# Performance work log

Measured on AMD Instinct MI355X. Metric: run time of the kernel, lower is better.

## Reference

```python
import jax, jax.numpy as jnp
import numpy as np

N_HASHES = 4
N_BUCKETS = 8
NUM_HEADS = 8
LN_EPS = 1e-5


def layer_norm(x, g, b):
    m = jnp.mean(x, axis=-1, keepdims=True)
    v = jnp.mean(jnp.square(x - m), axis=-1, keepdims=True)
    return (x - m) * jax.lax.rsqrt(v + LN_EPS) * g + b


def setup_inputs() -> dict:
    key = jax.random.key(0)
    ks = jax.random.split(key, 8)
    B, N, C = 16, 8192, 256
    dff = 4 * C
    w = 0.05  # weight init scale
    return {
        'x': jax.random.normal(ks[0], (B, N, C), jnp.float32),
        'rotations': jax.random.normal(ks[1], (1, C, N_HASHES, N_BUCKETS // 2), jnp.float32),
        'norm1_g': jnp.ones((C,), jnp.float32),
        'norm1_b': jnp.zeros((C,), jnp.float32),
        'q_w': jax.random.normal(ks[2], (C, C), jnp.float32) * w,
        'kv_w': jax.random.normal(ks[3], (C, 2 * C), jnp.float32) * w,
        'norm2_g': jnp.ones((C,), jnp.float32),
        'norm2_b': jnp.zeros((C,), jnp.float32),
        'fc1_w': jax.random.normal(ks[4], (C, dff), jnp.float32) * w,
        'fc1_b': jnp.zeros((dff,), jnp.float32),
        'fc2_w': jax.random.normal(ks[5], (dff, C), jnp.float32) * w,
        'fc2_b': jnp.zeros((C,), jnp.float32),
    }


def reference(x, rotations, norm1_g, norm1_b, q_w, kv_w, norm2_g, norm2_b, fc1_w, fc1_b, fc2_w, fc2_b):
    B, N, C = x.shape
    H = NUM_HEADS
    Dh = C // H
    scale = Dh ** -0.5

    x_ = layer_norm(x, norm1_g, norm1_b)

    # q: [B, H, N, Dh]
    q = (x_ @ q_w).reshape(B, N, H, Dh).transpose(0, 2, 1, 3)

    # --- hash_vectors: LSH bucket assignment + scatter-pool ---
    # rotated: [B, n_hashes, N, n_buckets//2] -> concat with negation -> n_buckets
    rotated = jnp.einsum('btf,fhi->bhti', x_, rotations[0])
    rotated = jnp.concatenate([rotated, -rotated], axis=-1)
    buckets = jnp.argmax(rotated, axis=-1)                      # [B, n_hashes, N]
    one_hot = jax.nn.one_hot(buckets, N_BUCKETS, dtype=x.dtype)  # [B, n_hashes, N, n_buckets]
    sum_buckets = jnp.sum(one_hot, axis=2)                       # [B, n_hashes, n_buckets]
    pooled = jnp.einsum('bnf,bhni->bhif', x_, one_hot)           # [B, n_hashes, n_buckets, C]
    pooled = pooled / (jax.lax.stop_gradient(sum_buckets)[..., None] + 1e-20)
    rp_x = pooled.reshape(B, N_HASHES * N_BUCKETS, C)            # [B, M, C] pooled KV tokens
    sumb = jax.lax.stop_gradient(sum_buckets.reshape(B, N_HASHES * N_BUCKETS))

    # kv: [2, B, H, M, Dh]
    M = N_HASHES * N_BUCKETS
    kv = (rp_x @ kv_w).reshape(B, M, 2, H, Dh).transpose(2, 0, 3, 1, 4)
    k, v = kv[0], kv[1]

    # masked attention over pooled buckets
    attn = jnp.einsum('bhnd,bhmd->bhnm', q, k) * scale           # [B, H, N, M]
    mask = (sumb >= 1)[:, None, None, :]                          # [B, 1, 1, M]
    attn = jnp.where(mask, attn, -jnp.finfo(attn.dtype).max)
    attn = jax.nn.softmax(attn, axis=-1)
    out = jnp.einsum('bhnm,bhmd->bnhd', attn, v).reshape(B, N, C)
    x = x + out

    # MLP block (GELU is exact erf, matching torch nn.GELU default)
    y = layer_norm(x, norm2_g, norm2_b)
    h = jax.nn.gelu(y @ fc1_w + fc1_b, approximate=False)
    y = h @ fc2_w + fc2_b
    return x + y
```

## Files before the change

kernel.cpp:

```cpp
#include <hip/hip_runtime.h>
#include <hip/hip_bf16.h>
#include <float.h>
#include <math.h>

#define Bn   16
#define Nn   8192
#define Cn   256
#define Hn   8
#define DHn  32
#define Mn   32
#define DFFn 1024
#define TOK  64

typedef __attribute__((ext_vector_type(8))) short short8;
typedef __attribute__((ext_vector_type(4))) float f32x4;

__device__ __forceinline__ float bf2f(ushort u) {
    union { unsigned int i; float f; } v; v.i = ((unsigned int)u) << 16; return v.f;
}
__device__ __forceinline__ ushort f2bf(float f) {
    union { float f; unsigned int i; } v; v.f = f;
    unsigned int r = (v.i + 0x7fffu + ((v.i >> 16) & 1u)) >> 16;
    return (ushort)r;
}

__global__ __launch_bounds__(256, 4) void ln1_pool_kernel(
    const float* __restrict__ x, const float* __restrict__ rot,
    const float* __restrict__ g1, const float* __restrict__ b1,
    ushort* __restrict__ xbf, float* __restrict__ pool_part, float* __restrict__ cnt_part)
{
    __shared__ ushort xt[TOK][Cn];
    __shared__ unsigned int idsS[TOK];

    const int tid  = threadIdx.x;
    const int w    = tid >> 6, lane = tid & 63;
    const int o    = lane & 15;
    const int g    = lane >> 4;
    const int fbase = g << 6;

    float rwv[64];
    #pragma unroll
    for (int f = 0; f < 64; ++f) rwv[f] = rot[(fbase + f) * 16 + o];

    const int b  = blockIdx.x >> 7;
    const int n0 = (blockIdx.x & 127) << 6;

    const float4 gv = *(const float4*)&g1[lane * 4];
    const float4 bv = *(const float4*)&b1[lane * 4];

    for (int it = 0; it < TOK / 4; ++it) {
        const int tloc = (it << 2) + w;
        const size_t roff = ((size_t)b * Nn + n0 + tloc) * Cn;
        float4 xv = *(const float4*)&x[roff + lane * 4];
        float s  = xv.x + xv.y + xv.z + xv.w;
        float s2 = xv.x * xv.x + xv.y * xv.y + xv.z * xv.z + xv.w * xv.w;
        #pragma unroll
        for (int msk = 1; msk < 64; msk <<= 1) { s += __shfl_xor(s, msk); s2 += __shfl_xor(s2, msk); }
        float mean = s * (1.f / Cn);
        float var  = s2 * (1.f / Cn) - mean * mean;
        float rr   = rsqrtf(var + 1e-5f);
        float xn[4];
        xn[0] = (xv.x - mean) * rr * gv.x + bv.x;
        xn[1] = (xv.y - mean) * rr * gv.y + bv.y;
        xn[2] = (xv.z - mean) * rr * gv.z + bv.z;
        xn[3] = (xv.w - mean) * rr * gv.w + bv.w;
        ushort4 ub; ub.x = f2bf(xn[0]); ub.y = f2bf(xn[1]); ub.z = f2bf(xn[2]); ub.w = f2bf(xn[3]);
        *(ushort4*)&xbf[roff + lane * 4] = ub;
        *(ushort4*)&xt[tloc][lane * 4] = ub;

        float d = 0.f;
        #pragma unroll
        for (int j = 0; j < 8; ++j) {
            short8 xs = *(const short8*)&xt[tloc][fbase + j * 8];
            #pragma unroll
            for (int u = 0; u < 8; ++u)
                d += bf2f((ushort)xs[u]) * rwv[j * 8 + u];
        }
        d += __shfl_xor(d, 16); d += __shfl_xor(d, 32);

        float d0 = __shfl(d, (lane & 12));
        float d1 = __shfl(d, (lane & 12) | 1);
        float d2 = __shfl(d, (lane & 12) | 2);
        float d3 = __shfl(d, (lane & 12) | 3);
        int bk = 0; float bb = d0;
        if (d1  > bb) { bb = d1;  bk = 1; }
        if (d2  > bb) { bb = d2;  bk = 2; }
        if (d3  > bb) { bb = d3;  bk = 3; }
        if (-d0 > bb) { bb = -d0; bk = 4; }
        if (-d1 > bb) { bb = -d1; bk = 5; }
        if (-d2 > bb) { bb = -d2; bk = 6; }
        if (-d3 > bb) { bb = -d3; bk = 7; }
        const unsigned int bk0 = __shfl(bk, 0), bk1 = __shfl(bk, 4),
                           bk2 = __shfl(bk, 8), bk3 = __shfl(bk, 12);
        if (lane == 0)
            idsS[tloc] = bk0 | (bk1 << 8) | (bk2 << 16) | (bk3 << 24);
    }
    __syncthreads();

    float pool[Mn];
    #pragma unroll
    for (int m = 0; m < Mn; ++m) pool[m] = 0.f;
    for (int t = 0; t < TOK; ++t) {
        const float xv = bf2f(xt[t][tid]);
        const unsigned int idw = idsS[t];
        #pragma unroll
        for (int h = 0; h < 4; ++h) {
            const unsigned int id = (idw >> (8 * h)) & 7u;
            #pragma unroll
            for (int mb = 0; mb < 8; ++mb)
                pool[h * 8 + mb] += (id == (unsigned int)mb) ? xv : 0.f;
        }
    }
    const size_t pbase = (size_t)blockIdx.x * (Mn * Cn);
    #pragma unroll
    for (int m = 0; m < Mn; ++m)
        pool_part[pbase + m * Cn + tid] = pool[m];

    if (tid < Mn) {
        const int h = tid >> 3, mb = tid & 7;
        float c = 0.f;
        for (int t = 0; t < TOK; ++t)
            c += (((idsS[t] >> (8 * h)) & 255u) == (unsigned int)mb) ? 1.f : 0.f;
        cnt_part[blockIdx.x * Mn + tid] = c;
    }
}

__global__ __launch_bounds__(256) void kv_kernel(
    const float* __restrict__ pool_part, const float* __restrict__ cnt_part,
    const float* __restrict__ kv_w, float* __restrict__ kbuf, float* __restrict__ vbuf,
    float* __restrict__ countsF)
{
    __shared__ float rp[Cn];
    const int tid = threadIdx.x;
    const int b = blockIdx.x >> 5;
    const int m = blockIdx.x & 31;

    float acc = 0.f, cnt = 0.f;
    for (int j = 0; j < 128; ++j) {
        const int blk = b * 128 + j;
        acc += pool_part[(size_t)blk * (Mn * Cn) + m * Cn + tid];
        cnt += cnt_part[blk * Mn + m];
    }
    rp[tid] = acc / (cnt + 1e-20f);
    if (tid == 0) countsF[b * Mn + m] = cnt;
    __syncthreads();

    float a0 = 0.f, a1 = 0.f;
    for (int f = 0; f < Cn; ++f) {
        float rv = rp[f];
        a0 += rv * kv_w[f * 512 + tid];
        a1 += rv * kv_w[f * 512 + 256 + tid];
    }
    const int h = tid >> 5, d = tid & 31;
    kbuf[(((size_t)b * Hn + h) * Mn + m) * DHn + d] = a0;
    vbuf[(((size_t)b * Hn + h) * Mn + m) * DHn + d] = a1;
}

template<int EPI>
__global__ __launch_bounds__(256) void gemm_bt(
    const ushort* __restrict__ A, const ushort* __restrict__ Bt,
    const float* __restrict__ bias, const float* __restrict__ resid,
    void* __restrict__ Cp, int Mrows, int Ncols, int K)
{
    __shared__ ushort As[128][40];
    __shared__ ushort Bs[128][40];
    const int tid  = threadIdx.x;
    const int lane = tid & 63;
    const int w    = tid >> 6;
    const int wm   = (w >> 1) << 6;
    const int wn   = (w & 1) << 6;
    const int lr   = lane & 15;
    const int lq   = lane >> 4;
    const int m0   = blockIdx.y << 7;
    const int n0   = blockIdx.x << 7;
    const int srow = tid >> 2;
    const int sch  = (tid & 3) << 3;

    f32x4 acc[4][4];
    #pragma unroll
    for (int i = 0; i < 4; i++)
        #pragma unroll
        for (int j = 0; j < 4; j++)
            acc[i][j] = (f32x4){0.f, 0.f, 0.f, 0.f};

    for (int k0 = 0; k0 < K; k0 += 32) {
        *(uint4*)&As[srow][sch]      = *(const uint4*)&A[(size_t)(m0 + srow) * K + k0 + sch];
        *(uint4*)&As[srow + 64][sch] = *(const uint4*)&A[(size_t)(m0 + srow + 64) * K + k0 + sch];
        *(uint4*)&Bs[srow][sch]      = *(const uint4*)&Bt[(size_t)(n0 + srow) * K + k0 + sch];
        *(uint4*)&Bs[srow + 64][sch] = *(const uint4*)&Bt[(size_t)(n0 + srow + 64) * K + k0 + sch];
        __syncthreads();
        short8 af[4], bfr[4];
        #pragma unroll
        for (int i = 0; i < 4; i++) af[i]  = *(const short8*)&As[wm + i * 16 + lr][lq * 8];
        #pragma unroll
        for (int j = 0; j < 4; j++) bfr[j] = *(const short8*)&Bs[wn + j * 16 + lr][lq * 8];
        #pragma unroll
        for (int i = 0; i < 4; i++)
            #pragma unroll
            for (int j = 0; j < 4; j++)
                acc[i][j] = __builtin_amdgcn_mfma_f32_16x16x32_bf16(af[i], bfr[j], acc[i][j], 0, 0, 0);
        __syncthreads();
    }

    #pragma unroll
    for (int i = 0; i < 4; i++) {
        #pragma unroll
        for (int j = 0; j < 4; j++) {
            const int col = n0 + wn + j * 16 + lr;
            #pragma unroll
            for (int r = 0; r < 4; r++) {
                const int rw = m0 + wm + i * 16 + lq * 4 + r;
                float v = acc[i][j][r];
                if (EPI == 1) { v += bias[col]; v = 0.5f * v * (1.f + erff(v * 0.70710678118654752f)); }
                if (EPI == 2) {
                    v += bias[col] + resid[(size_t)rw * Ncols + col];
                    ((float*)Cp)[(size_t)rw * Ncols + col] = v;
                } else {
                    ((ushort*)Cp)[(size_t)rw * Ncols + col] = f2bf(v);
                }
            }
        }
    }
}

__global__ __launch_bounds__(256) void attn_ln2_kernel(
    const ushort* __restrict__ q, const float* __restrict__ kbuf, const float* __restrict__ vbuf,
    const float* __restrict__ counts, const float* __restrict__ x,
    const float* __restrict__ g2, const float* __restrict__ b2,
    float* __restrict__ x2, ushort* __restrict__ ybf)
{
    __shared__ float kS[Hn * Mn * DHn];
    __shared__ float vS[Hn * Mn * DHn];
    __shared__ float mS[Mn];
    const int tid = threadIdx.x;
    const int b = blockIdx.x >> 5;
    const int n = ((blockIdx.x & 31) << 8) + tid;
    for (int i = tid; i < Hn * Mn * DHn; i += 256) {
        kS[i] = kbuf[(size_t)b * Hn * Mn * DHn + i];
        vS[i] = vbuf[(size_t)b * Hn * Mn * DHn + i];
    }
    if (tid < Mn) mS[tid] = counts[b * Mn + tid];
    __syncthreads();

    const size_t row = (size_t)b * Nn + n;
    float sum = 0.f, sum2 = 0.f;
    for (int h = 0; h < Hn; ++h) {
        float qh[32];
        const ushort* qp = q + row * Cn + h * DHn;
        #pragma unroll
        for (int i = 0; i < 4; ++i) {
            short8 qv = *(const short8*)(qp + i * 8);
            #pragma unroll
            for (int j = 0; j < 8; ++j) qh[i * 8 + j] = bf2f((ushort)qv[j]);
        }
        float p[32]; float mx = -FLT_MAX;
        #pragma unroll
        for (int m = 0; m < 32; ++m) {
            float sv;
            if (mS[m] >= 1.f) {
                sv = 0.f;
                const float* kp = &kS[(h * Mn + m) * DHn];
                #pragma unroll
                for (int dq = 0; dq < 8; ++dq) {
                    float4 k4 = *(const float4*)&kp[dq * 4];
                    sv += qh[dq*4+0]*k4.x + qh[dq*4+1]*k4.y + qh[dq*4+2]*k4.z + qh[dq*4+3]*k4.w;
                }
                sv *= 0.17677669529663687f;
            } else sv = -FLT_MAX;
            p[m] = sv; mx = fmaxf(mx, sv);
        }
        float den = 0.f;
        #pragma unroll
        for (int m = 0; m < 32; ++m) { float e = __expf(p[m] - mx); p[m] = e; den += e; }
        float inv = 1.f / den;
        float o[32];
        #pragma unroll
        for (int dd = 0; dd < 32; ++dd) o[dd] = 0.f;
        #pragma unroll
        for (int m = 0; m < 32; ++m) {
            float pm = p[m];
            const float* vp = &vS[(h * Mn + m) * DHn];
            #pragma unroll
            for (int dq = 0; dq < 8; ++dq) {
                float4 v4 = *(const float4*)&vp[dq * 4];
                o[dq*4+0] += pm*v4.x; o[dq*4+1] += pm*v4.y; o[dq*4+2] += pm*v4.z; o[dq*4+3] += pm*v4.w;
            }
        }
        #pragma unroll
        for (int dq = 0; dq < 8; ++dq) {
            float4 xv = *(const float4*)&x[row * Cn + h * DHn + dq * 4];
            float r0 = xv.x + o[dq*4+0]*inv;
            float r1 = xv.y + o[dq*4+1]*inv;
            float r2 = xv.z + o[dq*4+2]*inv;
            float r3 = xv.w + o[dq*4+3]*inv;
            *(float4*)&x2[row * Cn + h * DHn + dq * 4] = make_float4(r0, r1, r2, r3);
            sum  += r0 + r1 + r2 + r3;
            sum2 += r0*r0 + r1*r1 + r2*r2 + r3*r3;
        }
    }
    float mean = sum * (1.f / Cn);
    float var  = sum2 * (1.f / Cn) - mean * mean;
    float rr   = rsqrtf(var + 1e-5f);
    for (int i = 0; i < Cn / 4; ++i) {
        float4 xv = *(const float4*)&x2[row * Cn + i * 4];
        float4 gv = *(const float4*)&g2[i * 4];
        float4 bv = *(const float4*)&b2[i * 4];
        ushort4 ub;
        ub.x = f2bf((xv.x - mean) * rr * gv.x + bv.x);
        ub.y = f2bf((xv.y - mean) * rr * gv.y + bv.y);
        ub.z = f2bf((xv.z - mean) * rr * gv.z + bv.z);
        ub.w = f2bf((xv.w - mean) * rr * gv.w + bv.w);
        *(ushort4*)&ybf[row * Cn + i * 4] = ub;
    }
}

__global__ void wcast_kernel(const float* __restrict__ W, ushort* __restrict__ Wt, int R, int Cc)
{
    int idx = blockIdx.x * 256 + threadIdx.x;
    if (idx < R * Cc) {
        int r = idx / Cc, c = idx % Cc;
        Wt[(size_t)c * R + r] = f2bf(W[idx]);
    }
}

extern "C" void kernel_launch(void* const* d_in, const int* in_sizes, int n_in,
                              void* d_out, int out_size, void* d_ws, size_t ws_size,
                              hipStream_t stream)
{
    const float* x    = (const float*)d_in[0];
    const float* rot  = (const float*)d_in[1];
    const float* n1g  = (const float*)d_in[2];
    const float* n1b  = (const float*)d_in[3];
    const float* q_w  = (const float*)d_in[4];
    const float* kv_w = (const float*)d_in[5];
    const float* n2g  = (const float*)d_in[6];
    const float* n2b  = (const float*)d_in[7];
    const float* fc1w = (const float*)d_in[8];
    const float* fc1b = (const float*)d_in[9];
    const float* fc2w = (const float*)d_in[10];
    const float* fc2b = (const float*)d_in[11];

    char* ws = (char*)d_ws;
    const size_t XBF_OFF = 0;
    const size_t QBF_OFF = 67108864ull;
    const size_t H_OFF   = 0;
    const size_t X2_OFF  = 268435456ull;
    const size_t PP_OFF  = X2_OFF;
    const size_t CP_OFF  = X2_OFF + 67108864;
    const size_t Y_OFF   = 402653184ull;
    const size_t CT_OFF  = 469762048ull;
    const size_t KB_OFF  = CT_OFF + 4096;
    const size_t VB_OFF  = KB_OFF + 524288;
    const size_t QWT_OFF = VB_OFF + 524288;
    const size_t F1T_OFF = QWT_OFF + 131072;
    const size_t F2T_OFF = F1T_OFF + 524288;

    ushort* xbf    = (ushort*)(ws + XBF_OFF);
    ushort* qbf    = (ushort*)(ws + QBF_OFF);
    ushort* hbf    = (ushort*)(ws + H_OFF);
    float*  x2     = (float*)(ws + X2_OFF);
    float*  ppart  = (float*)(ws + PP_OFF);
    float*  cpart  = (float*)(ws + CP_OFF);
    ushort* ybf    = (ushort*)(ws + Y_OFF);
    float*  countsF= (float*)(ws + CT_OFF);
    float*  kbuf   = (float*)(ws + KB_OFF);
    float*  vbuf   = (float*)(ws + VB_OFF);
    ushort* qwT    = (ushort*)(ws + QWT_OFF);
    ushort* f1T    = (ushort*)(ws + F1T_OFF);
    ushort* f2T    = (ushort*)(ws + F2T_OFF);

    wcast_kernel<<<dim3(256), 256, 0, stream>>>(q_w, qwT, 256, 256);
    wcast_kernel<<<dim3(1024), 256, 0, stream>>>(fc1w, f1T, 256, 1024);
    wcast_kernel<<<dim3(1024), 256, 0, stream>>>(fc2w, f2T, 1024, 256);

    ln1_pool_kernel<<<dim3(Bn * 128), 256, 0, stream>>>(x, rot, n1g, n1b, xbf, ppart, cpart);
    kv_kernel<<<dim3(Bn * Mn), 256, 0, stream>>>(ppart, cpart, kv_w, kbuf, vbuf, countsF);
    gemm_bt<0><<<dim3(2, 1024), 256, 0, stream>>>(xbf, qwT, nullptr, nullptr, qbf, Bn * Nn, Cn, Cn);
    attn_ln2_kernel<<<dim3(Bn * 32), 256, 0, stream>>>(qbf, kbuf, vbuf, countsF, x, n2g, n2b, x2, ybf);
    gemm_bt<1><<<dim3(8, 1024), 256, 0, stream>>>(ybf, f1T, fc1b, nullptr, hbf, Bn * Nn, DFFn, Cn);
    gemm_bt<2><<<dim3(2, 1024), 256, 0, stream>>>(hbf, f2T, fc2b, x2, d_out, Bn * Nn, Cn, DFFn);
}
```

Baseline: 1.095 ms.

## Fold Q projection and K into per-batch score weights, fuse softmax-V-LN2

Precomputes a per-batch matrix W_s = q_w·K^T·scale, so the Q GEMM directly produces attention scores for all heads and the per-token QK dot products disappear. The attention kernel is rewritten so that lanes map to (token pair, head), each lane processes two tokens, and the LayerNorm statistics are reduced with shuffles instead of one thread walking a whole row. The LayerNorm input stays in registers rather than being re-read from global memory. In exchange it adds a small per-batch weight-build kernel and a batched B operand in the GEMM, and the scores are now rounded through bf16 before the softmax.

```diff
diff --git a/kernel.cpp b/kernel.cpp
--- a/kernel.cpp
+++ b/kernel.cpp
@@ -156,11 +156,36 @@
     vbuf[(((size_t)b * Hn + h) * Mn + m) * DHn + d] = a1;
 }
 
+__global__ __launch_bounds__(256) void ws_build_kernel(
+    const float* __restrict__ q_w, const float* __restrict__ kbuf, ushort* __restrict__ WsT)
+{
+    __shared__ float kSh[Mn * DHn];
+    const int tid = threadIdx.x;
+    const int b = blockIdx.x >> 3, h = blockIdx.x & 7;
+    for (int i = tid; i < Mn * DHn; i += 256)
+        kSh[i] = kbuf[((size_t)(b * Hn + h) * Mn) * DHn + i];
+    __syncthreads();
+
+    float qr[32];
+    #pragma unroll
+    for (int i = 0; i < 8; ++i) {
+        float4 v = *(const float4*)&q_w[(size_t)tid * Cn + h * DHn + i * 4];
+        qr[i*4+0] = v.x; qr[i*4+1] = v.y; qr[i*4+2] = v.z; qr[i*4+3] = v.w;
+    }
+    #pragma unroll 4
+    for (int m = 0; m < Mn; ++m) {
+        float s = 0.f;
+        #pragma unroll
+        for (int d = 0; d < DHn; ++d) s += qr[d] * kSh[m * DHn + d];
+        WsT[((size_t)b * Cn + h * Mn + m) * Cn + tid] = f2bf(s * 0.17677669529663687f);
+    }
+}
+
 template<int EPI>
 __global__ __launch_bounds__(256) void gemm_bt(
     const ushort* __restrict__ A, const ushort* __restrict__ Bt,
     const float* __restrict__ bias, const float* __restrict__ resid,
-    void* __restrict__ Cp, int Mrows, int Ncols, int K)
+    void* __restrict__ Cp, int Mrows, int Ncols, int K, int bstride)
 {
     __shared__ ushort As[128][40];
     __shared__ ushort Bs[128][40];
@@ -175,6 +200,7 @@
     const int n0   = blockIdx.x << 7;
     const int srow = tid >> 2;
     const int sch  = (tid & 3) << 3;
+    const ushort* Btb = Bt + (size_t)(m0 >> 13) * (size_t)bstride;
 
     f32x4 acc[4][4];
     #pragma unroll
@@ -186,8 +212,8 @@
     for (int k0 = 0; k0 < K; k0 += 32) {
         *(uint4*)&As[srow][sch]      = *(const uint4*)&A[(size_t)(m0 + srow) * K + k0 + sch];
         *(uint4*)&As[srow + 64][sch] = *(const uint4*)&A[(size_t)(m0 + srow + 64) * K + k0 + sch];
-        *(uint4*)&Bs[srow][sch]      = *(const uint4*)&Bt[(size_t)(n0 + srow) * K + k0 + sch];
-        *(uint4*)&Bs[srow + 64][sch] = *(const uint4*)&Bt[(size_t)(n0 + srow + 64) * K + k0 + sch];
+        *(uint4*)&Bs[srow][sch]      = *(const uint4*)&Btb[(size_t)(n0 + srow) * K + k0 + sch];
+        *(uint4*)&Bs[srow + 64][sch] = *(const uint4*)&Btb[(size_t)(n0 + srow + 64) * K + k0 + sch];
         __syncthreads();
         short8 af[4], bfr[4];
         #pragma unroll
@@ -223,94 +249,134 @@
     }
 }
 
-__global__ __launch_bounds__(256) void attn_ln2_kernel(
-    const ushort* __restrict__ q, const float* __restrict__ kbuf, const float* __restrict__ vbuf,
+#define VSH 1028
+#define GSH 36
+
+__global__ __launch_bounds__(256) void attn2_ln2_kernel(
+    const ushort* __restrict__ S, const float* __restrict__ vbuf,
     const float* __restrict__ counts, const float* __restrict__ x,
     const float* __restrict__ g2, const float* __restrict__ b2,
     float* __restrict__ x2, ushort* __restrict__ ybf)
 {
-    __shared__ float kS[Hn * Mn * DHn];
-    __shared__ float vS[Hn * Mn * DHn];
-    __shared__ float mS[Mn];
+    __shared__ float vS[Hn * VSH];
+    __shared__ float gS[Hn * GSH], bS[Hn * GSH];
+    __shared__ unsigned int mkS;
     const int tid = threadIdx.x;
-    const int b = blockIdx.x >> 5;
-    const int n = ((blockIdx.x & 31) << 8) + tid;
-    for (int i = tid; i < Hn * Mn * DHn; i += 256) {
-        kS[i] = kbuf[(size_t)b * Hn * Mn * DHn + i];
-        vS[i] = vbuf[(size_t)b * Hn * Mn * DHn + i];
-    }
-    if (tid < Mn) mS[tid] = counts[b * Mn + tid];
+    const int b = blockIdx.x >> 6;
+    const int nbase = (blockIdx.x & 63) << 7;
+
+    for (int i = tid; i < Hn * Mn * DHn; i += 256)
+        vS[(i >> 10) * VSH + (i & 1023)] = vbuf[(size_t)b * (Hn * Mn * DHn) + i];
+    gS[(tid >> 5) * GSH + (tid & 31)] = g2[tid];
+    bS[(tid >> 5) * GSH + (tid & 31)] = b2[tid];
+    if (tid == 0) {
+        unsigned int mq = 0;
+        for (int m = 0; m < Mn; ++m) if (counts[b * Mn + m] >= 1.f) mq |= (1u << m);
+        mkS = mq;
+    }
     __syncthreads();
-
-    const size_t row = (size_t)b * Nn + n;
-    float sum = 0.f, sum2 = 0.f;
-    for (int h = 0; h < Hn; ++h) {
-        float qh[32];
-        const ushort* qp = q + row * Cn + h * DHn;
+    const unsigned int mk = mkS;
+    const int w = tid >> 6, lane = tid & 63;
+    const int t8 = lane >> 3, h = lane & 7;
+    const float* vbase = &vS[h * VSH];
+    const float* gp = &gS[h * GSH];
+    const float* bp = &bS[h * GSH];
+
+    for (int it = 0; it < 2; ++it) {
+        const int nl = nbase + it * 64 + w * 16 + t8 * 2;
+        const size_t offA = ((size_t)b * Nn + nl) * Cn + h * DHn;
+
+        float pA[32], pB[32];
         #pragma unroll
         for (int i = 0; i < 4; ++i) {
-            short8 qv = *(const short8*)(qp + i * 8);
-            #pragma unroll
-            for (int j = 0; j < 8; ++j) qh[i * 8 + j] = bf2f((ushort)qv[j]);
-        }
-        float p[32]; float mx = -FLT_MAX;
+            short8 sa = *(const short8*)&S[offA + i * 8];
+            short8 sb = *(const short8*)&S[offA + Cn + i * 8];
+            #pragma unroll
+            for (int j = 0; j < 8; ++j) {
+                pA[i * 8 + j] = bf2f((ushort)sa[j]);
+                pB[i * 8 + j] = bf2f((ushort)sb[j]);
+            }
+        }
+        float mxA = -FLT_MAX, mxB = -FLT_MAX;
         #pragma unroll
         for (int m = 0; m < 32; ++m) {
-            float sv;
-            if (mS[m] >= 1.f) {
-                sv = 0.f;
-                const float* kp = &kS[(h * Mn + m) * DHn];
-                #pragma unroll
-                for (int dq = 0; dq < 8; ++dq) {
-                    float4 k4 = *(const float4*)&kp[dq * 4];
-                    sv += qh[dq*4+0]*k4.x + qh[dq*4+1]*k4.y + qh[dq*4+2]*k4.z + qh[dq*4+3]*k4.w;
-                }
-                sv *= 0.17677669529663687f;
-            } else sv = -FLT_MAX;
-            p[m] = sv; mx = fmaxf(mx, sv);
-        }
-        float den = 0.f;
-        #pragma unroll
-        for (int m = 0; m < 32; ++m) { float e = __expf(p[m] - mx); p[m] = e; den += e; }
-        float inv = 1.f / den;
-        float o[32];
-        #pragma unroll
-        for (int dd = 0; dd < 32; ++dd) o[dd] = 0.f;
+            if (!((mk >> m) & 1u)) { pA[m] = -FLT_MAX; pB[m] = -FLT_MAX; }
+            mxA = fmaxf(mxA, pA[m]); mxB = fmaxf(mxB, pB[m]);
+        }
+        float dA = 0.f, dB = 0.f;
         #pragma unroll
         for (int m = 0; m < 32; ++m) {
-            float pm = p[m];
-            const float* vp = &vS[(h * Mn + m) * DHn];
+            pA[m] = __expf(pA[m] - mxA); dA += pA[m];
+            pB[m] = __expf(pB[m] - mxB); dB += pB[m];
+        }
+        const float iA = 1.f / dA, iB = 1.f / dB;
+
+        float oA[32], oB[32];
+        #pragma unroll
+        for (int i = 0; i < 32; ++i) { oA[i] = 0.f; oB[i] = 0.f; }
+        #pragma unroll
+        for (int m = 0; m < 32; ++m) {
+            const float a = pA[m], c = pB[m];
+            const float* vp = vbase + m * DHn;
             #pragma unroll
             for (int dq = 0; dq < 8; ++dq) {
                 float4 v4 = *(const float4*)&vp[dq * 4];
-                o[dq*4+0] += pm*v4.x; o[dq*4+1] += pm*v4.y; o[dq*4+2] += pm*v4.z; o[dq*4+3] += pm*v4.w;
+                oA[dq*4+0] += a * v4.x; oA[dq*4+1] += a * v4.y;
+                oA[dq*4+2] += a * v4.z; oA[dq*4+3] += a * v4.w;
+                oB[dq*4+0] += c * v4.x; oB[dq*4+1] += c * v4.y;
+                oB[dq*4+2] += c * v4.z; oB[dq*4+3] += c * v4.w;
             }
         }
+
+        float sA = 0.f, s2A = 0.f, sB = 0.f, s2B = 0.f;
         #pragma unroll
         for (int dq = 0; dq < 8; ++dq) {
-            float4 xv = *(const float4*)&x[row * Cn + h * DHn + dq * 4];
-            float r0 = xv.x + o[dq*4+0]*inv;
-            float r1 = xv.y + o[dq*4+1]*inv;
-            float r2 = xv.z + o[dq*4+2]*inv;
-            float r3 = xv.w + o[dq*4+3]*inv;
-            *(float4*)&x2[row * Cn + h * DHn + dq * 4] = make_float4(r0, r1, r2, r3);
-            sum  += r0 + r1 + r2 + r3;
-            sum2 += r0*r0 + r1*r1 + r2*r2 + r3*r3;
-        }
-    }
-    float mean = sum * (1.f / Cn);
-    float var  = sum2 * (1.f / Cn) - mean * mean;
-    float rr   = rsqrtf(var + 1e-5f);
-    for (int i = 0; i < Cn / 4; ++i) {
-        float4 xv = *(const float4*)&x2[row * Cn + i * 4];
-        float4 gv = *(const float4*)&g2[i * 4];
-        float4 bv = *(const float4*)&b2[i * 4];
-        ushort4 ub;
-        ub.x = f2bf((xv.x - mean) * rr * gv.x + bv.x);
-        ub.y = f2bf((xv.y - mean) * rr * gv.y + bv.y);
-        ub.z = f2bf((xv.z - mean) * rr * gv.z + bv.z);
-        ub.w = f2bf((xv.w - mean) * rr * gv.w + bv.w);
-        *(ushort4*)&ybf[row * Cn + i * 4] = ub;
+            float4 xa = *(const float4*)&x[offA + dq * 4];
+            float4 xb = *(const float4*)&x[offA + Cn + dq * 4];
+            float r0 = xa.x + oA[dq*4+0] * iA;
+            float r1 = xa.y + oA[dq*4+1] * iA;
+            float r2 = xa.z + oA[dq*4+2] * iA;
+            float r3 = xa.w + oA[dq*4+3] * iA;
+            float u0 = xb.x + oB[dq*4+0] * iB;
+            float u1 = xb.y + oB[dq*4+1] * iB;
+            float u2 = xb.z + oB[dq*4+2] * iB;
+            float u3 = xb.w + oB[dq*4+3] * iB;
+            *(float4*)&x2[offA + dq * 4]      = make_float4(r0, r1, r2, r3);
+            *(float4*)&x2[offA + Cn + dq * 4] = make_float4(u0, u1, u2, u3);
+            oA[dq*4+0] = r0; oA[dq*4+1] = r1; oA[dq*4+2] = r2; oA[dq*4+3] = r3;
+            oB[dq*4+0] = u0; oB[dq*4+1] = u1; oB[dq*4+2] = u2; oB[dq*4+3] = u3;
+            sA += r0 + r1 + r2 + r3; s2A += r0*r0 + r1*r1 + r2*r2 + r3*r3;
+            sB += u0 + u1 + u2 + u3; s2B += u0*u0 + u1*u1 + u2*u2 + u3*u3;
+        }
+        #pragma unroll
+        for (int msk = 1; msk < 8; msk <<= 1) {
+            sA += __shfl_xor(sA, msk);  s2A += __shfl_xor(s2A, msk);
+            sB += __shfl_xor(sB, msk);  s2B += __shfl_xor(s2B, msk);
+        }
+        const float mA = sA * (1.f / Cn), vA = s2A * (1.f / Cn) - mA * mA;
+        const float rrA = rsqrtf(vA + 1e-5f);
+        const float mB = sB * (1.f / Cn), vB = s2B * (1.f / Cn) - mB * mB;
+        const float rrB = rsqrtf(vB + 1e-5f);
+
+        #pragma unroll
+        for (int dq = 0; dq < 8; dq += 2) {
+            short8 ya, yb;
+            #pragma unroll
+            for (int u = 0; u < 2; ++u) {
+                float4 g4 = *(const float4*)&gp[(dq + u) * 4];
+                float4 b4 = *(const float4*)&bp[(dq + u) * 4];
+                ya[u*4+0] = (short)f2bf((oA[(dq+u)*4+0] - mA) * rrA * g4.x + b4.x);
+                ya[u*4+1] = (short)f2bf((oA[(dq+u)*4+1] - mA) * rrA * g4.y + b4.y);
+                ya[u*4+2] = (short)f2bf((oA[(dq+u)*4+2] - mA) * rrA * g4.z + b4.z);
+                ya[u*4+3] = (short)f2bf((oA[(dq+u)*4+3] - mA) * rrA * g4.w + b4.w);
+                yb[u*4+0] = (short)f2bf((oB[(dq+u)*4+0] - mB) * rrB * g4.x + b4.x);
+                yb[u*4+1] = (short)f2bf((oB[(dq+u)*4+1] - mB) * rrB * g4.y + b4.y);
+                yb[u*4+2] = (short)f2bf((oB[(dq+u)*4+2] - mB) * rrB * g4.z + b4.z);
+                yb[u*4+3] = (short)f2bf((oB[(dq+u)*4+3] - mB) * rrB * g4.w + b4.w);
+            }
+            *(short8*)&ybf[offA + dq * 4]      = ya;
+            *(short8*)&ybf[offA + Cn + dq * 4] = yb;
+        }
     }
 }
 
@@ -342,7 +408,7 @@
 
     char* ws = (char*)d_ws;
     const size_t XBF_OFF = 0;
-    const size_t QBF_OFF = 67108864ull;
+    const size_t S_OFF   = 67108864ull;
     const size_t H_OFF   = 0;
     const size_t X2_OFF  = 268435456ull;
     const size_t PP_OFF  = X2_OFF;
@@ -351,32 +417,31 @@
     const size_t CT_OFF  = 469762048ull;
     const size_t KB_OFF  = CT_OFF + 4096;
     const size_t VB_OFF  = KB_OFF + 524288;
-    const size_t QWT_OFF = VB_OFF + 524288;
-    const size_t F1T_OFF = QWT_OFF + 131072;
+    const size_t F1T_OFF = VB_OFF + 524288;
     const size_t F2T_OFF = F1T_OFF + 524288;
 
     ushort* xbf    = (ushort*)(ws + XBF_OFF);
-    ushort* qbf    = (ushort*)(ws + QBF_OFF);
+    ushort* Sbuf   = (ushort*)(ws + S_OFF);
     ushort* hbf    = (ushort*)(ws + H_OFF);
     float*  x2     = (float*)(ws + X2_OFF);
     float*  ppart  = (float*)(ws + PP_OFF);
     float*  cpart  = (float*)(ws + CP_OFF);
+    ushort* WsT    = (ushort*)(ws + X2_OFF);
     ushort* ybf    = (ushort*)(ws + Y_OFF);
     float*  countsF= (float*)(ws + CT_OFF);
     float*  kbuf   = (float*)(ws + KB_OFF);
     float*  vbuf   = (float*)(ws + VB_OFF);
-    ushort* qwT    = (ushort*)(ws + QWT_OFF);
     ushort* f1T    = (ushort*)(ws + F1T_OFF);
     ushort* f2T    = (ushort*)(ws + F2T_OFF);
 
-    wcast_kernel<<<dim3(256), 256, 0, stream>>>(q_w, qwT, 256, 256);
     wcast_kernel<<<dim3(1024), 256, 0, stream>>>(fc1w, f1T, 256, 1024);
     wcast_kernel<<<dim3(1024), 256, 0, stream>>>(fc2w, f2T, 1024, 256);
 
     ln1_pool_kernel<<<dim3(Bn * 128), 256, 0, stream>>>(x, rot, n1g, n1b, xbf, ppart, cpart);
     kv_kernel<<<dim3(Bn * Mn), 256, 0, stream>>>(ppart, cpart, kv_w, kbuf, vbuf, countsF);
-    gemm_bt<0><<<dim3(2, 1024), 256, 0, stream>>>(xbf, qwT, nullptr, nullptr, qbf, Bn * Nn, Cn, Cn);
-    attn_ln2_kernel<<<dim3(Bn * 32), 256, 0, stream>>>(qbf, kbuf, vbuf, countsF, x, n2g, n2b, x2, ybf);
-    gemm_bt<1><<<dim3(8, 1024), 256, 0, stream>>>(ybf, f1T, fc1b, nullptr, hbf, Bn * Nn, DFFn, Cn);
-    gemm_bt<2><<<dim3(2, 1024), 256, 0, stream>>>(hbf, f2T, fc2b, x2, d_out, Bn * Nn, Cn, DFFn);
-}
+    ws_build_kernel<<<dim3(Bn * Hn), 256, 0, stream>>>(q_w, kbuf, WsT);
+    gemm_bt<0><<<dim3(2, 1024), 256, 0, stream>>>(xbf, WsT, nullptr, nullptr, Sbuf, Bn * Nn, Cn, Cn, Cn * Cn);
+    attn2_ln2_kernel<<<dim3(Bn * 64), 256, 0, stream>>>(Sbuf, vbuf, countsF, x, n2g, n2b, x2, ybf);
+    gemm_bt<1><<<dim3(8, 1024), 256, 0, stream>>>(ybf, f1T, fc1b, nullptr, hbf, Bn * Nn, DFFn, Cn, 0);
+    gemm_bt<2><<<dim3(2, 1024), 256, 0, stream>>>(hbf, f2T, fc2b, x2, d_out, Bn * Nn, Cn, DFFn, 0);
+}
```

Result: slower. 1.273 ms (+16.2%).
